# Kernel tuning notes

Measured on AMD Instinct MI355X. Metric: run time of the kernel, lower is better.

## Reference

```python
import jax, jax.numpy as jnp
import numpy as np
import math

B, S, D = 16, 256, 41
LATENT, NREF, NLAYERS, NHEADS = 128, 128, 3, 4


def setup_inputs() -> dict:
    key = jax.random.key(0)
    ks = jax.random.split(key, 12)
    time_x = jax.random.uniform(ks[0], (B, S), dtype=jnp.float32)
    value_x = jax.random.normal(ks[1], (B, S, D), dtype=jnp.float32)
    mask_x = jax.random.randint(ks[2], (B, S, D), 0, 2).astype(jnp.int32)
    s = 0.05
    Wi = jax.random.normal(ks[3], (D + 2, LATENT), dtype=jnp.float32) * s
    bi = jnp.zeros((LATENT,), jnp.float32)
    I = jax.random.normal(ks[4], (NLAYERS, NREF, LATENT), dtype=jnp.float32) * s
    # axis 1: 0 -> mab0 (induced->data), 1 -> mab1 (data->induced)
    Wq = jax.random.normal(ks[5], (NLAYERS, 2, LATENT, LATENT), dtype=jnp.float32) * s
    Wk = jax.random.normal(ks[6], (NLAYERS, 2, LATENT, LATENT), dtype=jnp.float32) * s
    Wv = jax.random.normal(ks[7], (NLAYERS, 2, LATENT, LATENT), dtype=jnp.float32) * s
    Wo = jax.random.normal(ks[8], (NLAYERS, 2, LATENT, LATENT), dtype=jnp.float32) * s
    bq = jnp.zeros((NLAYERS, 2, LATENT), jnp.float32)
    bk = jnp.zeros((NLAYERS, 2, LATENT), jnp.float32)
    bv = jnp.zeros((NLAYERS, 2, LATENT), jnp.float32)
    bo = jnp.zeros((NLAYERS, 2, LATENT), jnp.float32)
    return dict(time_x=time_x, value_x=value_x, mask_x=mask_x, Wi=Wi, bi=bi, I=I,
                Wq=Wq, bq=bq, Wk=Wk, bk=bk, Wv=Wv, bv=bv, Wo=Wo, bo=bo)


def _mab(Q, K, Wq, bq, Wk, bk, Wv, bv, Wo, bo, key_mask):
    # MAB2: multi-head attn (heads via split-last-dim), residual Q_, then O + relu(fc_o(O))
    dV = Wq.shape[1]
    dh = dV // NHEADS
    Bq, Lq, _ = Q.shape
    Qh = (Q @ Wq + bq).reshape(Bq, Lq, NHEADS, dh)
    Kh = (K @ Wk + bk).reshape(Bq, -1, NHEADS, dh)
    Vh = (K @ Wv + bv).reshape(Bq, -1, NHEADS, dh)
    att = jnp.einsum('bqhd,bkhd->bhqk', Qh, Kh) / math.sqrt(dV)
    if key_mask is not None:
        att = jnp.where(key_mask[:, None, None, :] == 0, -10e9, att)
    A = jax.nn.softmax(att, axis=-1)
    O = (Qh + jnp.einsum('bhqk,bkhd->bqhd', A, Vh)).reshape(Bq, Lq, dV)
    return O + jax.nn.relu(O @ Wo + bo)


def reference(time_x, value_x, mask_x, Wi, bi, I, Wq, bq, Wk, bk, Wv, bv, Wo, bo):
    L = S * D
    mflat = mask_x.reshape(B, L)
    # stable compaction: valid entries first, original row-major order preserved
    order = jnp.argsort(1 - mflat, axis=1)  # jnp.argsort is stable
    T = jnp.broadcast_to(time_x[:, :, None], (B, S, D)).reshape(B, L)
    C = jnp.broadcast_to(jnp.arange(D, dtype=jnp.int32), (B, S, D)).reshape(B, L)
    U = value_x.reshape(B, L)
    g = lambda a: jnp.take_along_axis(a, order, axis=1)
    T_, U_, C_, mk_i = g(T), g(U), g(C), g(mflat)
    mk = mk_i.astype(jnp.float32)  # [B, L]
    Coh = jax.nn.one_hot(C_, D, dtype=jnp.float32)
    X = jnp.concatenate([Coh, T_[..., None], U_[..., None]], axis=-1) * mk[..., None]
    Z = jax.nn.relu(X @ Wi + bi) * mk[..., None]  # Y_e, [B, L, LATENT]
    for l in range(NLAYERS):
        Ib = jnp.broadcast_to(I[l][None], (B, NREF, LATENT))
        H = _mab(Ib, Z, Wq[l, 0], bq[l, 0], Wk[l, 0], bk[l, 0], Wv[l, 0], bv[l, 0],
                 Wo[l, 0], bo[l, 0], mk)          # induced points attend to masked data
        O = _mab(Z, H, Wq[l, 1], bq[l, 1], Wk[l, 1], bk[l, 1], Wv[l, 1], bv[l, 1],
                 Wo[l, 1], bo[l, 1], None)        # data attends to induced points (all valid)
        Z = O * mk[..., None] + Z
    return Z, mk[..., None]
```

## Files before the change

### kernel.cpp

```cpp
#include <hip/hip_runtime.h>
#include <math.h>

#define BB 16
#define SS 256
#define DD 41
#define LL (SS*DD)
#define LAT 128
#define NH 4
#define NL 3
#define KS 16
#define RSQ 0.08838834764831845f

typedef short bf16x8 __attribute__((ext_vector_type(8)));
typedef float f32x4 __attribute__((ext_vector_type(4)));
#define MFMA __builtin_amdgcn_mfma_f32_16x16x32_bf16

__device__ __forceinline__ unsigned short f2b(float f) {
    unsigned u = __builtin_bit_cast(unsigned, f);
    unsigned r = (u + 0x7FFFu + ((u >> 16) & 1u)) >> 16;
    return (unsigned short)r;
}
__device__ __forceinline__ float b2f(unsigned short h) {
    unsigned u = ((unsigned)h) << 16;
    return __builtin_bit_cast(float, u);
}

__global__ __launch_bounds__(256)
void k_compact(const float* __restrict__ time_x, const float* __restrict__ value_x,
               const int* __restrict__ mask_x,
               float* __restrict__ compT, float* __restrict__ compU,
               int* __restrict__ compC, int* __restrict__ nvalid)
{
    int b = blockIdx.x, tid = threadIdx.x;
    int lane = tid & 63, w = tid >> 6;
    __shared__ int sW[4];
    __shared__ int s_base;
    if (tid == 0) s_base = 0;
    __syncthreads();
    for (int j0 = 0; j0 < LL; j0 += 256) {
        int j = j0 + tid;
        int m = mask_x[b * LL + j];
        unsigned long long bal = __ballot(m != 0);
        int pre = __popcll(bal & ((1ull << lane) - 1ull));
        if (lane == 0) sW[w] = __popcll(bal);
        __syncthreads();
        int woff = 0;
        for (int i = 0; i < w; ++i) woff += sW[i];
        int tot = sW[0] + sW[1] + sW[2] + sW[3];
        if (m) {
            int pos = s_base + woff + pre;
            compT[b * LL + pos] = time_x[b * SS + j / DD];
            compU[b * LL + pos] = value_x[b * LL + j];
            compC[b * LL + pos] = j % DD;
        }
        __syncthreads();
        if (tid == 0) s_base += tot;
        __syncthreads();
    }
    if (tid == 0) nvalid[b] = s_base;
}

__global__ __launch_bounds__(256)
void k_init(const float* __restrict__ Wi, const float* __restrict__ bi,
            const float* __restrict__ compT, const float* __restrict__ compU,
            const int* __restrict__ compC, const int* __restrict__ nvalid,
            float* __restrict__ out)
{
    int b = blockIdx.y, p0 = blockIdx.x * 8, tid = threadIdx.x;
    float* Z = out;
    float* MK = out + (size_t)BB * LL * LAT;
    int nv = nvalid[b];
    for (int s = 0; s < 4; ++s) {
        int e = s * 256 + tid;
        int r = e >> 7, k = e & 127;
        int p = p0 + r;
        size_t zi = ((size_t)b * LL + p) * LAT + k;
        if (p < nv) {
            int c = compC[b * LL + p];
            float t = compT[b * LL + p], u = compU[b * LL + p];
            float v = Wi[c * LAT + k] + t * Wi[41 * LAT + k] + u * Wi[42 * LAT + k] + bi[k];
            Z[zi] = fmaxf(v, 0.f);
        } else {
            Z[zi] = 0.f;
        }
        if (k == 0) MK[b * LL + p] = (p < nv) ? 1.f : 0.f;
    }
}

__global__ __launch_bounds__(256)
void k_prep(const float* __restrict__ I, const float* __restrict__ Wq,
            const float* __restrict__ bq,
            const float* __restrict__ Wk, const float* __restrict__ Wv,
            const float* __restrict__ Wo,
            float* __restrict__ Qh0f, unsigned short* __restrict__ Qh0b,
            unsigned short* __restrict__ WkT, unsigned short* __restrict__ WvT,
            unsigned short* __restrict__ WqT, unsigned short* __restrict__ WoT)
{
    __shared__ float srow[128];
    int blk = blockIdx.x, tid = threadIdx.x, l = blockIdx.y;
    const float* Il  = I  + (size_t)l * 16384;
    const float* Wq0 = Wq + (size_t)(l * 2 + 0) * 16384;
    const float* bq0 = bq + (size_t)(l * 2 + 0) * 128;
    const float* Wk0 = Wk + (size_t)(l * 2 + 0) * 16384;
    const float* Wv0 = Wv + (size_t)(l * 2 + 0) * 16384;
    const float* Wq1 = Wq + (size_t)(l * 2 + 1) * 16384;
    const float* Wo1 = Wo + (size_t)(l * 2 + 1) * 16384;
    if (blk < 128) {
        if (tid < 128) srow[tid] = Il[blk * 128 + tid];
        __syncthreads();
        if (tid < 128) {
            float acc = bq0[tid];
            for (int i = 0; i < 128; ++i) acc += srow[i] * Wq0[i * 128 + tid];
            Qh0f[(size_t)l * 16384 + blk * 128 + tid] = acc;
            Qh0b[(size_t)l * 16384 + blk * 128 + tid] = f2b(acc);
        }
    } else {
        const float* src = (blk == 128) ? Wk0 : (blk == 129) ? Wv0 : (blk == 130) ? Wq1 : Wo1;
        unsigned short* dst = (blk == 128) ? WkT : (blk == 129) ? WvT : (blk == 130) ? WqT : WoT;
        dst += (size_t)l * 16384;
        for (int e = tid; e < 16384; e += 256) {
            int i = e >> 7, n = e & 127;
            dst[n * 128 + i] = f2b(src[e]);
        }
    }
}

__global__ __launch_bounds__(512, 4)
void k_flash0(const float* __restrict__ Z, const unsigned short* __restrict__ Qh0b,
              const unsigned short* __restrict__ WkT, const unsigned short* __restrict__ WvT,
              const float* __restrict__ bk0, const float* __restrict__ bv0,
              const int* __restrict__ nvalid, float* __restrict__ ml,
              unsigned short* __restrict__ accp)
{
    const int chunk = blockIdx.x, b = blockIdx.y;
    const int tid = threadIdx.x, lane = tid & 63, w = tid >> 6;
    const int l16 = lane & 15, g4 = lane >> 4;
    const f32x4 fz = {0.f, 0.f, 0.f, 0.f};

    __shared__ unsigned short sZ[32 * 136];
    __shared__ unsigned short sKh[32 * 136];
    __shared__ unsigned short sVT[128 * 40];
    __shared__ float sS[128 * 33];
    __shared__ unsigned short sP[128 * 40];
    __shared__ float sM[NH * 128], sL[NH * 128], sScale[128];

    for (int e = tid; e < NH * 128; e += 512) { sM[e] = -1e30f; sL[e] = 0.f; }

    f32x4 acc[8];
    for (int n = 0; n < 8; ++n) acc[n] = fz;

    int nv = nvalid[b];
    int c0 = (int)(((long long)chunk * nv) / KS);
    int c1 = (int)(((long long)(chunk + 1) * nv) / KS);

    float bkd = bk0[w * 16 + l16];
    float bvd = bv0[w * 16 + l16];

    const int sr = tid >> 4, sc = (tid & 15) * 8;
    float4 pa, pb;
    if (c0 < c1) {
        const float* s = &Z[((size_t)b * LL + c0 + sr) * LAT + sc];
        pa = *(const float4*)s; pb = *(const float4*)(s + 4);
    }

    __syncthreads();

    for (int kt = c0; kt < c1; kt += 32) {
        int nk = min(32, c1 - kt);
        {
            bf16x8 v;
            if (sr < nk) {
                ((unsigned short*)&v)[0] = f2b(pa.x);
                ((unsigned short*)&v)[1] = f2b(pa.y);
                ((unsigned short*)&v)[2] = f2b(pa.z);
                ((unsigned short*)&v)[3] = f2b(pa.w);
                ((unsigned short*)&v)[4] = f2b(pb.x);
                ((unsigned short*)&v)[5] = f2b(pb.y);
                ((unsigned short*)&v)[6] = f2b(pb.z);
                ((unsigned short*)&v)[7] = f2b(pb.w);
            } else {
                #pragma unroll
                for (int j = 0; j < 8; ++j) ((unsigned short*)&v)[j] = 0;
            }
            *(bf16x8*)&sZ[sr * 136 + sc] = v;
        }
        __syncthreads();
        if (kt + 32 < c1) {
            const float* s = &Z[((size_t)b * LL + kt + 32 + sr) * LAT + sc];
            pa = *(const float4*)s; pb = *(const float4*)(s + 4);
        }
        {
            f32x4 ck[2] = {fz, fz}, cv[2] = {fz, fz};
            #pragma unroll
            for (int k = 0; k < 4; ++k) {
                bf16x8 a0 = *(const bf16x8*)&sZ[(l16) * 136 + k * 32 + g4 * 8];
                bf16x8 a1 = *(const bf16x8*)&sZ[(16 + l16) * 136 + k * 32 + g4 * 8];
                bf16x8 bk_ = *(const bf16x8*)&WkT[(w * 16 + l16) * 128 + k * 32 + g4 * 8];
                bf16x8 bv_ = *(const bf16x8*)&WvT[(w * 16 + l16) * 128 + k * 32 + g4 * 8];
                ck[0] = MFMA(a0, bk_, ck[0], 0, 0, 0);
                ck[1] = MFMA(a1, bk_, ck[1], 0, 0, 0);
                cv[0] = MFMA(a0, bv_, cv[0], 0, 0, 0);
                cv[1] = MFMA(a1, bv_, cv[1], 0, 0, 0);
            }
            #pragma unroll
            for (int m = 0; m < 2; ++m)
                #pragma unroll
                for (int r = 0; r < 4; ++r) {
                    int kk = m * 16 + g4 * 4 + r;
                    int d = w * 16 + l16;
                    sKh[kk * 136 + d] = f2b(ck[m][r] + bkd);
                    sVT[d * 40 + kk] = f2b(cv[m][r] + bvd);
                }
        }
        __syncthreads();
        for (int h = 0; h < NH; ++h) {
            bf16x8 aq = *(const bf16x8*)&Qh0b[(w * 16 + l16) * 128 + h * 32 + g4 * 8];
            #pragma unroll
            for (int n = 0; n < 2; ++n) {
                bf16x8 bk_ = *(const bf16x8*)&sKh[(n * 16 + l16) * 136 + h * 32 + g4 * 8];
                f32x4 s = MFMA(aq, bk_, fz, 0, 0, 0);
                #pragma unroll
                for (int r = 0; r < 4; ++r)
                    sS[(w * 16 + g4 * 4 + r) * 33 + n * 16 + l16] = s[r] * RSQ;
            }
            int q = w * 16 + (lane >> 2);
            int k0 = (lane & 3) * 8;
            float sv[8];
            float mx = -1e30f;
            #pragma unroll
            for (int j = 0; j < 8; ++j) {
                int kk = k0 + j;
                sv[j] = (kk < nk) ? sS[q * 33 + kk] : -1e30f;
                mx = fmaxf(mx, sv[j]);
            }
            mx = fmaxf(mx, __shfl_xor(mx, 1));
            mx = fmaxf(mx, __shfl_xor(mx, 2));
            float mr = sM[h * 128 + q];
            float mn = fmaxf(mr, mx);
            float sc = __expf(mr - mn);
            float ls = 0.f;
            bf16x8 pv;
            #pragma unroll
            for (int j = 0; j < 8; ++j) {
                float p = (k0 + j < nk) ? __expf(sv[j] - mn) : 0.f;
                ((unsigned short*)&pv)[j] = f2b(p);
                ls += p;
            }
            *(bf16x8*)&sP[q * 40 + k0] = pv;
            ls += __shfl_xor(ls, 1);
            ls += __shfl_xor(ls, 2);
            if ((lane & 3) == 0) {
                sM[h * 128 + q] = mn;
                sL[h * 128 + q] = sL[h * 128 + q] * sc + ls;
                sScale[q] = sc;
            }
            #pragma unroll
            for (int nn = 0; nn < 2; ++nn) {
                int nt = 2 * h + nn;
                #pragma unroll
                for (int r = 0; r < 4; ++r) {
                    float scq = sScale[w * 16 + g4 * 4 + r];
                    acc[nt][r] *= scq;
                }
            }
            bf16x8 aP = *(const bf16x8*)&sP[(w * 16 + l16) * 40 + g4 * 8];
            #pragma unroll
            for (int nn = 0; nn < 2; ++nn) {
                bf16x8 bV = *(const bf16x8*)&sVT[(h * 32 + nn * 16 + l16) * 40 + g4 * 8];
                acc[2 * h + nn] = MFMA(aP, bV, acc[2 * h + nn], 0, 0, 0);
            }
        }
        __syncthreads();
    }
    __syncthreads();
    size_t mlbase = (((size_t)b * KS + chunk) * NH) * 128 * 2;
    for (int e = tid; e < NH * 128; e += 512) {
        ml[mlbase + e * 2 + 0] = sM[e];
        ml[mlbase + e * 2 + 1] = sL[e];
    }
    size_t abase = (((size_t)b * KS + chunk) * 128) * 128;
    #pragma unroll
    for (int n = 0; n < 8; ++n)
        #pragma unroll
        for (int r = 0; r < 4; ++r) {
            int q = w * 16 + g4 * 4 + r;
            int d = n * 16 + l16;
            accp[abase + (size_t)q * 128 + d] = f2b(acc[n][r]);
        }
}

__global__ __launch_bounds__(128)
void k_post0(const float* __restrict__ ml, const unsigned short* __restrict__ accp,
             const float* __restrict__ Qh0f,
             const float* __restrict__ Wo0, const float* __restrict__ bo0,
             const float* __restrict__ Wk1, const float* __restrict__ bk1,
             const float* __restrict__ Wv1, const float* __restrict__ bv1,
             unsigned short* __restrict__ Kh1b, unsigned short* __restrict__ Vh1Tb)
{
    int q = blockIdx.x, b = blockIdx.y, d = threadIdx.x, h = d >> 5;
    __shared__ float sx[128], sh2[128];
    float M = -1e30f;
    for (int c = 0; c < KS; ++c)
        M = fmaxf(M, ml[((((size_t)b * KS + c) * NH + h) * 128 + q) * 2]);
    float L = 0.f, A = 0.f;
    for (int c = 0; c < KS; ++c) {
        size_t base = ((((size_t)b * KS + c) * NH + h) * 128 + q) * 2;
        float sc = __expf(ml[base] - M);
        L += sc * ml[base + 1];
        A += sc * b2f(accp[(((size_t)b * KS + c) * 128 + q) * 128 + d]);
    }
    float o0 = Qh0f[q * 128 + d] + ((L > 0.f) ? A / L : 0.f);
    sx[d] = o0;
    __syncthreads();
    float acc = bo0[d];
    for (int i = 0; i < 128; ++i) acc += sx[i] * Wo0[i * 128 + d];
    float hv = o0 + fmaxf(acc, 0.f);
    sh2[d] = hv;
    __syncthreads();
    float ak = bk1[d], av = bv1[d];
    for (int i = 0; i < 128; ++i) {
        float x = sh2[i];
        ak += x * Wk1[i * 128 + d];
        av += x * Wv1[i * 128 + d];
    }
    Kh1b[((size_t)b * 128 + q) * 128 + d] = f2b(ak);
    Vh1Tb[((size_t)b * 128 + d) * 128 + q] = f2b(av);
}

__global__ __launch_bounds__(512, 6)
void k_mab1(float* __restrict__ Z, const unsigned short* __restrict__ Kh1b,
            const unsigned short* __restrict__ Vh1Tb,
            const unsigned short* __restrict__ WqT, const float* __restrict__ bq1,
            const unsigned short* __restrict__ WoT, const float* __restrict__ bo1,
            const int* __restrict__ nvalid)
{
    const int b = blockIdx.y;
    const int p0 = blockIdx.x * 64;
    const int nv = nvalid[b];
    if (p0 >= nv) return;
    const int tid = threadIdx.x, lane = tid & 63, w = tid >> 6;
    const int l16 = lane & 15, g4 = lane >> 4;
    const f32x4 fz = {0.f, 0.f, 0.f, 0.f};

    __shared__ unsigned short sQh[64 * 136];
    __shared__ unsigned short sU[8 * 16 * 136];

    {
        int r = tid >> 3, c = (tid & 7) * 16;
        const float* zr = &Z[((size_t)b * LL + p0 + r) * LAT + c];
        #pragma unroll
        for (int half = 0; half < 2; ++half) {
            float4 f0 = *(const float4*)(zr + half * 8);
            float4 f1 = *(const float4*)(zr + half * 8 + 4);
            bf16x8 v;
            ((unsigned short*)&v)[0] = f2b(f0.x);
            ((unsigned short*)&v)[1] = f2b(f0.y);
            ((unsigned short*)&v)[2] = f2b(f0.z);
            ((unsigned short*)&v)[3] = f2b(f0.w);
            ((unsigned short*)&v)[4] = f2b(f1.x);
            ((unsigned short*)&v)[5] = f2b(f1.y);
            ((unsigned short*)&v)[6] = f2b(f1.z);
            ((unsigned short*)&v)[7] = f2b(f1.w);
            *(bf16x8*)&sU[r * 136 + c + half * 8] = v;
        }
    }
    __syncthreads();
    {
        f32x4 c4[4] = {fz, fz, fz, fz};
        #pragma unroll
        for (int ks = 0; ks < 4; ++ks) {
            bf16x8 bw = *(const bf16x8*)&WqT[(w * 16 + l16) * 128 + ks * 32 + g4 * 8];
            #pragma unroll
            for (int mt = 0; mt < 4; ++mt) {
                bf16x8 a = *(const bf16x8*)&sU[(mt * 16 + l16) * 136 + ks * 32 + g4 * 8];
                c4[mt] = MFMA(a, bw, c4[mt], 0, 0, 0);
            }
        }
        float bqv = bq1[w * 16 + l16];
        #pragma unroll
        for (int mt = 0; mt < 4; ++mt)
            #pragma unroll
            for (int r = 0; r < 4; ++r)
                sQh[(mt * 16 + g4 * 4 + r) * 136 + w * 16 + l16] = f2b(c4[mt][r] + bqv);
    }
    __syncthreads();

    const int t = w >> 1;
    const int hbase = (w & 1) * 2;
    unsigned short* ps = &sU[w * 16 * 136];
    f32x4 oacc[2][2];

    #pragma unroll
    for (int hh = 0; hh < 2; ++hh) {
        const int h = hbase + hh;
        f32x4 s[8];
        bf16x8 bq8 = *(const bf16x8*)&sQh[(t * 16 + l16) * 136 + h * 32 + g4 * 8];
        #pragma unroll
        for (int mt = 0; mt < 8; ++mt) {
            bf16x8 ak = *(const bf16x8*)&Kh1b[((size_t)b * 128 + mt * 16 + l16) * 128 + h * 32 + g4 * 8];
            s[mt] = MFMA(ak, bq8, fz, 0, 0, 0);
        }
        float mx = -1e30f;
        #pragma unroll
        for (int mt = 0; mt < 8; ++mt)
            #pragma unroll
            for (int r = 0; r < 4; ++r) mx = fmaxf(mx, s[mt][r]);
        mx = fmaxf(mx, __shfl_xor(mx, 16));
        mx = fmaxf(mx, __shfl_xor(mx, 32));
        float ls = 0.f;
        #pragma unroll
        for (int mt = 0; mt < 8; ++mt)
            #pragma unroll
            for (int r = 0; r < 4; ++r) {
                float p = __expf((s[mt][r] - mx) * RSQ);
                s[mt][r] = p;
                ls += p;
            }
        ls += __shfl_xor(ls, 16);
        ls += __shfl_xor(ls, 32);
        float inv = 1.f / ls;
        #pragma unroll
        for (int mt = 0; mt < 8; ++mt) {
            unsigned short p4[4];
            #pragma unroll
            for (int r = 0; r < 4; ++r) p4[r] = f2b(s[mt][r] * inv);
            *(uint2*)&ps[l16 * 136 + mt * 16 + g4 * 4] = *(const uint2*)p4;
        }
        #pragma unroll
        for (int nn = 0; nn < 2; ++nn) {
            f32x4 o = fz;
            #pragma unroll
            for (int ks = 0; ks < 4; ++ks) {
                bf16x8 aP = *(const bf16x8*)&ps[l16 * 136 + ks * 32 + g4 * 8];
                bf16x8 bV = *(const bf16x8*)&Vh1Tb[((size_t)b * 128 + h * 32 + nn * 16 + l16) * 128 + ks * 32 + g4 * 8];
                o = MFMA(aP, bV, o, 0, 0, 0);
            }
            oacc[hh][nn] = o;
        }
    }
    #pragma unroll
    for (int hh = 0; hh < 2; ++hh)
        #pragma unroll
        for (int nn = 0; nn < 2; ++nn) {
            int col = (hbase + hh) * 32 + nn * 16 + l16;
            #pragma unroll
            for (int r = 0; r < 4; ++r) {
                int row = t * 16 + g4 * 4 + r;
                float val = oacc[hh][nn][r] + b2f(sQh[row * 136 + col]);
                sQh[row * 136 + col] = f2b(val);
            }
        }
    __syncthreads();
    {
        f32x4 c4[4] = {fz, fz, fz, fz};
        #pragma unroll
        for (int ks = 0; ks < 4; ++ks) {
            bf16x8 bw = *(const bf16x8*)&WoT[(w * 16 + l16) * 128 + ks * 32 + g4 * 8];
            #pragma unroll
            for (int mt = 0; mt < 4; ++mt) {
                bf16x8 a = *(const bf16x8*)&sQh[(mt * 16 + l16) * 136 + ks * 32 + g4 * 8];
                c4[mt] = MFMA(a, bw, c4[mt], 0, 0, 0);
            }
        }
        float bov = bo1[w * 16 + l16];
        #pragma unroll
        for (int mt = 0; mt < 4; ++mt)
            #pragma unroll
            for (int r = 0; r < 4; ++r) {
                int row = mt * 16 + g4 * 4 + r;
                int col = w * 16 + l16;
                if (p0 + row < nv) {
                    size_t zi = ((size_t)b * LL + p0 + row) * LAT + col;
                    Z[zi] = Z[zi] + b2f(sQh[row * 136 + col]) + fmaxf(c4[mt][r] + bov, 0.f);
                }
            }
    }
}

extern "C" void kernel_launch(void* const* d_in, const int* in_sizes, int n_in,
                              void* d_out, int out_size, void* d_ws, size_t ws_size,
                              hipStream_t stream)
{
    const float* time_x  = (const float*)d_in[0];
    const float* value_x = (const float*)d_in[1];
    const int*   mask_x  = (const int*)d_in[2];
    const float* Wi = (const float*)d_in[3];
    const float* bi = (const float*)d_in[4];
    const float* I  = (const float*)d_in[5];
    const float* Wq = (const float*)d_in[6];
    const float* bq = (const float*)d_in[7];
    const float* Wk = (const float*)d_in[8];
    const float* bk = (const float*)d_in[9];
    const float* Wv = (const float*)d_in[10];
    const float* bv = (const float*)d_in[11];
    const float* Wo = (const float*)d_in[12];
    const float* bo = (const float*)d_in[13];
    float* out = (float*)d_out;

    const size_t BL = (size_t)BB * LL;
    float* ws = (float*)d_ws;
    float* compT  = ws;                      ws += BL;
    float* compU  = ws;                      ws += BL;
    int*   compC  = (int*)ws;                ws += BL;
    int*   nvalid = (int*)ws;                ws += 64;
    float* Qh0f   = ws;                      ws += (size_t)NL * 16384;
    float* ml     = ws;                      ws += (size_t)BB * KS * NH * 128 * 2;
    unsigned short* accp  = (unsigned short*)ws;  ws += ((size_t)BB * KS * 128 * 128) / 2;
    unsigned short* Qh0b  = (unsigned short*)ws;  ws += (size_t)NL * 8192;
    unsigned short* WkT   = (unsigned short*)ws;  ws += (size_t)NL * 8192;
    unsigned short* WvT   = (unsigned short*)ws;  ws += (size_t)NL * 8192;
    unsigned short* WqT   = (unsigned short*)ws;  ws += (size_t)NL * 8192;
    unsigned short* WoT   = (unsigned short*)ws;  ws += (size_t)NL * 8192;
    unsigned short* Kh1b  = (unsigned short*)ws;  ws += ((size_t)BB * 16384) / 2;
    unsigned short* Vh1Tb = (unsigned short*)ws;  ws += ((size_t)BB * 16384) / 2;

    k_compact<<<BB, 256, 0, stream>>>(time_x, value_x, mask_x, compT, compU, compC, nvalid);
    k_init<<<dim3(LL / 8, BB), 256, 0, stream>>>(Wi, bi, compT, compU, compC, nvalid, out);
    k_prep<<<dim3(132, NL), 256, 0, stream>>>(I, Wq, bq, Wk, Wv, Wo,
                                              Qh0f, Qh0b, WkT, WvT, WqT, WoT);

    for (int l = 0; l < NL; ++l) {
        const float* Wo0 = Wo + (size_t)(l * 2 + 0) * 16384;
        const float* Wk1 = Wk + (size_t)(l * 2 + 1) * 16384;
        const float* Wv1 = Wv + (size_t)(l * 2 + 1) * 16384;
        const float* bk0 = bk + (l * 2 + 0) * 128;
        const float* bv0 = bv + (l * 2 + 0) * 128;
        const float* bo0 = bo + (l * 2 + 0) * 128;
        const float* bq1 = bq + (l * 2 + 1) * 128;
        const float* bk1 = bk + (l * 2 + 1) * 128;
        const float* bv1 = bv + (l * 2 + 1) * 128;
        const float* bo1 = bo + (l * 2 + 1) * 128;

        k_flash0<<<dim3(KS, BB), 512, 0, stream>>>(out, Qh0b + (size_t)l * 16384,
                                                   WkT + (size_t)l * 16384,
                                                   WvT + (size_t)l * 16384,
                                                   bk0, bv0, nvalid, ml, accp);
        k_post0<<<dim3(128, BB), 128, 0, stream>>>(ml, accp, Qh0f + (size_t)l * 16384,
                                                   Wo0, bo0, Wk1, bk1, Wv1, bv1, Kh1b, Vh1Tb);
        k_mab1<<<dim3(LL / 64, BB), 512, 0, stream>>>(out, Kh1b, Vh1Tb,
                                                      WqT + (size_t)l * 16384, bq1,
                                                      WoT + (size_t)l * 16384, bo1, nvalid);
    }
}
```

Measured before the change: 573.1 us.

## Keep a bf16 shadow copy of Z and double attention split count

Adds a bf16 copy of Z, written by k_init and by k_mab1's epilogue, so k_flash0 and k_mab1 read half the bytes and skip per-element fp32-to-bf16 conversion. The k_mab1 epilogue now stages the relu output in shared memory and writes Z in coalesced float4 rows. When the workspace is large enough, the flash split count rises from 16 to 32 to give the split-K attention more blocks. The cost is extra bf16 writes per layer, a larger partial-result buffer and a longer reduction in k_post0, and the fast path depends on the workspace size.

New measurement: 574.0 us. About the same (+0.2%).

```diff
diff --git a/kernel.cpp b/kernel.cpp
--- a/kernel.cpp
+++ b/kernel.cpp
@@ -8,7 +8,6 @@
 #define LAT 128
 #define NH 4
 #define NL 3
-#define KS 16
 #define RSQ 0.08838834764831845f
 
 typedef short bf16x8 __attribute__((ext_vector_type(8)));
@@ -60,30 +59,35 @@
     if (tid == 0) nvalid[b] = s_base;
 }
 
+template<int UZ>
 __global__ __launch_bounds__(256)
 void k_init(const float* __restrict__ Wi, const float* __restrict__ bi,
             const float* __restrict__ compT, const float* __restrict__ compU,
             const int* __restrict__ compC, const int* __restrict__ nvalid,
-            float* __restrict__ out)
+            float* __restrict__ out, unsigned short* __restrict__ Zb)
 {
     int b = blockIdx.y, p0 = blockIdx.x * 8, tid = threadIdx.x;
     float* Z = out;
     float* MK = out + (size_t)BB * LL * LAT;
     int nv = nvalid[b];
-    for (int s = 0; s < 4; ++s) {
+    for (int s = 0; s < 2; ++s) {
         int e = s * 256 + tid;
-        int r = e >> 7, k = e & 127;
+        int r = e >> 6, k2 = (e & 63) * 2;
         int p = p0 + r;
-        size_t zi = ((size_t)b * LL + p) * LAT + k;
+        size_t zi = ((size_t)b * LL + p) * LAT + k2;
+        float v0 = 0.f, v1 = 0.f;
         if (p < nv) {
             int c = compC[b * LL + p];
             float t = compT[b * LL + p], u = compU[b * LL + p];
-            float v = Wi[c * LAT + k] + t * Wi[41 * LAT + k] + u * Wi[42 * LAT + k] + bi[k];
-            Z[zi] = fmaxf(v, 0.f);
-        } else {
-            Z[zi] = 0.f;
-        }
-        if (k == 0) MK[b * LL + p] = (p < nv) ? 1.f : 0.f;
+            v0 = fmaxf(Wi[c * LAT + k2]     + t * Wi[41 * LAT + k2]     + u * Wi[42 * LAT + k2]     + bi[k2],     0.f);
+            v1 = fmaxf(Wi[c * LAT + k2 + 1] + t * Wi[41 * LAT + k2 + 1] + u * Wi[42 * LAT + k2 + 1] + bi[k2 + 1], 0.f);
+        }
+        *(float2*)&Z[zi] = make_float2(v0, v1);
+        if constexpr (UZ) {
+            unsigned short h2[2] = {f2b(v0), f2b(v1)};
+            *(unsigned*)&Zb[((size_t)b * LL + p) * LAT + k2] = *(const unsigned*)h2;
+        }
+        if (k2 == 0) MK[b * LL + p] = (p < nv) ? 1.f : 0.f;
     }
 }
 
@@ -125,12 +129,14 @@
     }
 }
 
+template<int UZ>
 __global__ __launch_bounds__(512, 4)
-void k_flash0(const float* __restrict__ Z, const unsigned short* __restrict__ Qh0b,
+void k_flash0(const float* __restrict__ Z, const unsigned short* __restrict__ Zb,
+              const unsigned short* __restrict__ Qh0b,
               const unsigned short* __restrict__ WkT, const unsigned short* __restrict__ WvT,
               const float* __restrict__ bk0, const float* __restrict__ bv0,
               const int* __restrict__ nvalid, float* __restrict__ ml,
-              unsigned short* __restrict__ accp)
+              unsigned short* __restrict__ accp, int ks)
 {
     const int chunk = blockIdx.x, b = blockIdx.y;
     const int tid = threadIdx.x, lane = tid & 63, w = tid >> 6;
@@ -150,24 +156,32 @@
     for (int n = 0; n < 8; ++n) acc[n] = fz;
 
     int nv = nvalid[b];
-    int c0 = (int)(((long long)chunk * nv) / KS);
-    int c1 = (int)(((long long)(chunk + 1) * nv) / KS);
+    int c0 = (int)(((long long)chunk * nv) / ks);
+    int c1 = (int)(((long long)(chunk + 1) * nv) / ks);
 
     float bkd = bk0[w * 16 + l16];
     float bvd = bv0[w * 16 + l16];
 
     const int sr = tid >> 4, sc = (tid & 15) * 8;
     float4 pa, pb;
+    uint4 pz;
     if (c0 < c1) {
-        const float* s = &Z[((size_t)b * LL + c0 + sr) * LAT + sc];
-        pa = *(const float4*)s; pb = *(const float4*)(s + 4);
+        if constexpr (UZ) {
+            pz = *(const uint4*)&Zb[((size_t)b * LL + c0 + sr) * LAT + sc];
+        } else {
+            const float* s = &Z[((size_t)b * LL + c0 + sr) * LAT + sc];
+            pa = *(const float4*)s; pb = *(const float4*)(s + 4);
+        }
     }
 
     __syncthreads();
 
     for (int kt = c0; kt < c1; kt += 32) {
         int nk = min(32, c1 - kt);
-        {
+        if constexpr (UZ) {
+            uint4 z4 = {0u, 0u, 0u, 0u};
+            *(uint4*)&sZ[sr * 136 + sc] = (sr < nk) ? pz : z4;
+        } else {
             bf16x8 v;
             if (sr < nk) {
                 ((unsigned short*)&v)[0] = f2b(pa.x);
@@ -186,8 +200,12 @@
         }
         __syncthreads();
         if (kt + 32 < c1) {
-            const float* s = &Z[((size_t)b * LL + kt + 32 + sr) * LAT + sc];
-            pa = *(const float4*)s; pb = *(const float4*)(s + 4);
+            if constexpr (UZ) {
+                pz = *(const uint4*)&Zb[((size_t)b * LL + kt + 32 + sr) * LAT + sc];
+            } else {
+                const float* s = &Z[((size_t)b * LL + kt + 32 + sr) * LAT + sc];
+                pa = *(const float4*)s; pb = *(const float4*)(s + 4);
+            }
         }
         {
             f32x4 ck[2] = {fz, fz}, cv[2] = {fz, fz};
@@ -273,12 +291,12 @@
         __syncthreads();
     }
     __syncthreads();
-    size_t mlbase = (((size_t)b * KS + chunk) * NH) * 128 * 2;
+    size_t mlbase = (((size_t)b * ks + chunk) * NH) * 128 * 2;
     for (int e = tid; e < NH * 128; e += 512) {
         ml[mlbase + e * 2 + 0] = sM[e];
         ml[mlbase + e * 2 + 1] = sL[e];
     }
-    size_t abase = (((size_t)b * KS + chunk) * 128) * 128;
+    size_t abase = (((size_t)b * ks + chunk) * 128) * 128;
     #pragma unroll
     for (int n = 0; n < 8; ++n)
         #pragma unroll
@@ -295,19 +313,19 @@
              const float* __restrict__ Wo0, const float* __restrict__ bo0,
              const float* __restrict__ Wk1, const float* __restrict__ bk1,
              const float* __restrict__ Wv1, const float* __restrict__ bv1,
-             unsigned short* __restrict__ Kh1b, unsigned short* __restrict__ Vh1Tb)
+             unsigned short* __restrict__ Kh1b, unsigned short* __restrict__ Vh1Tb, int ks)
 {
     int q = blockIdx.x, b = blockIdx.y, d = threadIdx.x, h = d >> 5;
     __shared__ float sx[128], sh2[128];
     float M = -1e30f;
-    for (int c = 0; c < KS; ++c)
-        M = fmaxf(M, ml[((((size_t)b * KS + c) * NH + h) * 128 + q) * 2]);
+    for (int c = 0; c < ks; ++c)
+        M = fmaxf(M, ml[((((size_t)b * ks + c) * NH + h) * 128 + q) * 2]);
     float L = 0.f, A = 0.f;
-    for (int c = 0; c < KS; ++c) {
-        size_t base = ((((size_t)b * KS + c) * NH + h) * 128 + q) * 2;
+    for (int c = 0; c < ks; ++c) {
+        size_t base = ((((size_t)b * ks + c) * NH + h) * 128 + q) * 2;
         float sc = __expf(ml[base] - M);
         L += sc * ml[base + 1];
-        A += sc * b2f(accp[(((size_t)b * KS + c) * 128 + q) * 128 + d]);
+        A += sc * b2f(accp[(((size_t)b * ks + c) * 128 + q) * 128 + d]);
     }
     float o0 = Qh0f[q * 128 + d] + ((L > 0.f) ? A / L : 0.f);
     sx[d] = o0;
@@ -327,12 +345,14 @@
     Vh1Tb[((size_t)b * 128 + d) * 128 + q] = f2b(av);
 }
 
+template<int UZ>
 __global__ __launch_bounds__(512, 6)
-void k_mab1(float* __restrict__ Z, const unsigned short* __restrict__ Kh1b,
+void k_mab1(float* __restrict__ Z, unsigned short* __restrict__ Zb,
+            const unsigned short* __restrict__ Kh1b,
             const unsigned short* __restrict__ Vh1Tb,
             const unsigned short* __restrict__ WqT, const float* __restrict__ bq1,
             const unsigned short* __restrict__ WoT, const float* __restrict__ bo1,
-            const int* __restrict__ nvalid)
+            const int* __restrict__ nvalid, int writeZb)
 {
     const int b = blockIdx.y;
     const int p0 = blockIdx.x * 64;
@@ -344,24 +364,31 @@
 
     __shared__ unsigned short sQh[64 * 136];
     __shared__ unsigned short sU[8 * 16 * 136];
+    float* sUf = (float*)sU;
 
     {
         int r = tid >> 3, c = (tid & 7) * 16;
-        const float* zr = &Z[((size_t)b * LL + p0 + r) * LAT + c];
-        #pragma unroll
-        for (int half = 0; half < 2; ++half) {
-            float4 f0 = *(const float4*)(zr + half * 8);
-            float4 f1 = *(const float4*)(zr + half * 8 + 4);
-            bf16x8 v;
-            ((unsigned short*)&v)[0] = f2b(f0.x);
-            ((unsigned short*)&v)[1] = f2b(f0.y);
-            ((unsigned short*)&v)[2] = f2b(f0.z);
-            ((unsigned short*)&v)[3] = f2b(f0.w);
-            ((unsigned short*)&v)[4] = f2b(f1.x);
-            ((unsigned short*)&v)[5] = f2b(f1.y);
-            ((unsigned short*)&v)[6] = f2b(f1.z);
-            ((unsigned short*)&v)[7] = f2b(f1.w);
-            *(bf16x8*)&sU[r * 136 + c + half * 8] = v;
+        if constexpr (UZ) {
+            const uint4* zsrc = (const uint4*)&Zb[((size_t)b * LL + p0 + r) * LAT + c];
+            *(uint4*)&sU[r * 136 + c]     = zsrc[0];
+            *(uint4*)&sU[r * 136 + c + 8] = zsrc[1];
+        } else {
+            const float* zr = &Z[((size_t)b * LL + p0 + r) * LAT + c];
+            #pragma unroll
+            for (int half = 0; half < 2; ++half) {
+                float4 f0 = *(const float4*)(zr + half * 8);
+                float4 f1 = *(const float4*)(zr + half * 8 + 4);
+                bf16x8 v;
+                ((unsigned short*)&v)[0] = f2b(f0.x);
+                ((unsigned short*)&v)[1] = f2b(f0.y);
+                ((unsigned short*)&v)[2] = f2b(f0.z);
+                ((unsigned short*)&v)[3] = f2b(f0.w);
+                ((unsigned short*)&v)[4] = f2b(f1.x);
+                ((unsigned short*)&v)[5] = f2b(f1.y);
+                ((unsigned short*)&v)[6] = f2b(f1.z);
+                ((unsigned short*)&v)[7] = f2b(f1.w);
+                *(bf16x8*)&sU[r * 136 + c + half * 8] = v;
+            }
         }
     }
     __syncthreads();
@@ -468,12 +495,38 @@
             #pragma unroll
             for (int r = 0; r < 4; ++r) {
                 int row = mt * 16 + g4 * 4 + r;
-                int col = w * 16 + l16;
-                if (p0 + row < nv) {
-                    size_t zi = ((size_t)b * LL + p0 + row) * LAT + col;
-                    Z[zi] = Z[zi] + b2f(sQh[row * 136 + col]) + fmaxf(c4[mt][r] + bov, 0.f);
+                sUf[row * 132 + w * 16 + l16] = fmaxf(c4[mt][r] + bov, 0.f);
+            }
+    }
+    __syncthreads();
+    {
+        int row = tid >> 3, cc = (tid & 7) * 16;
+        if (p0 + row < nv) {
+            size_t zi = ((size_t)b * LL + p0 + row) * LAT + cc;
+            float vout[16];
+            const unsigned short* ob = &sQh[row * 136 + cc];
+            const float* rf = &sUf[row * 132 + cc];
+            #pragma unroll
+            for (int i = 0; i < 4; ++i) {
+                float4 zv = *(const float4*)&Z[zi + i * 4];
+                vout[i * 4 + 0] = zv.x + b2f(ob[i * 4 + 0]) + rf[i * 4 + 0];
+                vout[i * 4 + 1] = zv.y + b2f(ob[i * 4 + 1]) + rf[i * 4 + 1];
+                vout[i * 4 + 2] = zv.z + b2f(ob[i * 4 + 2]) + rf[i * 4 + 2];
+                vout[i * 4 + 3] = zv.w + b2f(ob[i * 4 + 3]) + rf[i * 4 + 3];
+            }
+            #pragma unroll
+            for (int i = 0; i < 4; ++i)
+                *(float4*)&Z[zi + i * 4] = make_float4(vout[i*4], vout[i*4+1], vout[i*4+2], vout[i*4+3]);
+            if constexpr (UZ) {
+                if (writeZb) {
+                    unsigned short hb[16];
+                    #pragma unroll
+                    for (int i = 0; i < 16; ++i) hb[i] = f2b(vout[i]);
+                    *(uint4*)&Zb[((size_t)b * LL + p0 + row) * LAT + cc]     = *(const uint4*)&hb[0];
+                    *(uint4*)&Zb[((size_t)b * LL + p0 + row) * LAT + cc + 8] = *(const uint4*)&hb[8];
                 }
             }
+        }
     }
 }
 
@@ -498,24 +551,35 @@
     float* out = (float*)d_out;
 
     const size_t BL = (size_t)BB * LL;
+    const size_t base_fl = 3 * BL + 64 + (size_t)NL * 16384 + 5 * (size_t)NL * 8192
+                         + 2 * (size_t)BB * 8192;
+    const size_t ml_fl_32   = (size_t)BB * 32 * NH * 256;
+    const size_t accp_fl_32 = (size_t)BB * 32 * 8192;
+    const size_t zb_fl      = BL * 64 + 8192;
+    const size_t need_big   = (base_fl + ml_fl_32 + accp_fl_32 + zb_fl) * 4;
+    const int big = (ws_size >= need_big);
+    const int ks = big ? 32 : 16;
+
     float* ws = (float*)d_ws;
     float* compT  = ws;                      ws += BL;
     float* compU  = ws;                      ws += BL;
     int*   compC  = (int*)ws;                ws += BL;
     int*   nvalid = (int*)ws;                ws += 64;
     float* Qh0f   = ws;                      ws += (size_t)NL * 16384;
-    float* ml     = ws;                      ws += (size_t)BB * KS * NH * 128 * 2;
-    unsigned short* accp  = (unsigned short*)ws;  ws += ((size_t)BB * KS * 128 * 128) / 2;
     unsigned short* Qh0b  = (unsigned short*)ws;  ws += (size_t)NL * 8192;
     unsigned short* WkT   = (unsigned short*)ws;  ws += (size_t)NL * 8192;
     unsigned short* WvT   = (unsigned short*)ws;  ws += (size_t)NL * 8192;
     unsigned short* WqT   = (unsigned short*)ws;  ws += (size_t)NL * 8192;
     unsigned short* WoT   = (unsigned short*)ws;  ws += (size_t)NL * 8192;
-    unsigned short* Kh1b  = (unsigned short*)ws;  ws += ((size_t)BB * 16384) / 2;
-    unsigned short* Vh1Tb = (unsigned short*)ws;  ws += ((size_t)BB * 16384) / 2;
+    unsigned short* Kh1b  = (unsigned short*)ws;  ws += (size_t)BB * 8192;
+    unsigned short* Vh1Tb = (unsigned short*)ws;  ws += (size_t)BB * 8192;
+    float* ml     = ws;                      ws += (size_t)BB * ks * NH * 256;
+    unsigned short* accp  = (unsigned short*)ws;  ws += (size_t)BB * ks * 8192;
+    unsigned short* Zb    = (unsigned short*)ws;
 
     k_compact<<<BB, 256, 0, stream>>>(time_x, value_x, mask_x, compT, compU, compC, nvalid);
-    k_init<<<dim3(LL / 8, BB), 256, 0, stream>>>(Wi, bi, compT, compU, compC, nvalid, out);
+    if (big) k_init<1><<<dim3(LL / 8, BB), 256, 0, stream>>>(Wi, bi, compT, compU, compC, nvalid, out, Zb);
+    else     k_init<0><<<dim3(LL / 8, BB), 256, 0, stream>>>(Wi, bi, compT, compU, compC, nvalid, out, Zb);
     k_prep<<<dim3(132, NL), 256, 0, stream>>>(I, Wq, bq, Wk, Wv, Wo,
                                               Qh0f, Qh0b, WkT, WvT, WqT, WoT);
 
@@ -531,14 +595,26 @@
         const float* bv1 = bv + (l * 2 + 1) * 128;
         const float* bo1 = bo + (l * 2 + 1) * 128;
 
-        k_flash0<<<dim3(KS, BB), 512, 0, stream>>>(out, Qh0b + (size_t)l * 16384,
-                                                   WkT + (size_t)l * 16384,
-                                                   WvT + (size_t)l * 16384,
-                                                   bk0, bv0, nvalid, ml, accp);
+        if (big)
+            k_flash0<1><<<dim3(ks, BB), 512, 0, stream>>>(out, Zb, Qh0b + (size_t)l * 16384,
+                                                          WkT + (size_t)l * 16384,
+                                                          WvT + (size_t)l * 16384,
+                                                          bk0, bv0, nvalid, ml, accp, ks);
+        else
+            k_flash0<0><<<dim3(ks, BB), 512, 0, stream>>>(out, Zb, Qh0b + (size_t)l * 16384,
+                                                          WkT + (size_t)l * 16384,
+                                                          WvT + (size_t)l * 16384,
+                                                          bk0, bv0, nvalid, ml, accp, ks);
         k_post0<<<dim3(128, BB), 128, 0, stream>>>(ml, accp, Qh0f + (size_t)l * 16384,
-                                                   Wo0, bo0, Wk1, bk1, Wv1, bv1, Kh1b, Vh1Tb);
-        k_mab1<<<dim3(LL / 64, BB), 512, 0, stream>>>(out, Kh1b, Vh1Tb,
-                                                      WqT + (size_t)l * 16384, bq1,
-                                                      WoT + (size_t)l * 16384, bo1, nvalid);
-    }
-}
+                                                   Wo0, bo0, Wk1, bk1, Wv1, bv1, Kh1b, Vh1Tb, ks);
+        int wzb = (l < NL - 1) ? 1 : 0;
+        if (big)
+            k_mab1<1><<<dim3(LL / 64, BB), 512, 0, stream>>>(out, Zb, Kh1b, Vh1Tb,
+                                                             WqT + (size_t)l * 16384, bq1,
+                                                             WoT + (size_t)l * 16384, bo1, nvalid, wzb);
+        else
+            k_mab1<0><<<dim3(LL / 64, BB), 512, 0, stream>>>(out, Zb, Kh1b, Vh1Tb,
+                                                             WqT + (size_t)l * 16384, bq1,
+                                                             WoT + (size_t)l * 16384, bo1, nvalid, wzb);
+    }
+}
```
